# Kernel optimization log

Hardware: AMD Instinct MI355X
Metric: run time of the kernel (lower is better)

The kernel has to match this reference:

```python
import jax, jax.numpy as jnp
import numpy as np

N = 20000      # nodes
E = 640000     # edges
FIN = 256
FQK = 256


def setup_inputs() -> dict:
    key = jax.random.key(0)
    kx, ks, kd, kw = jax.random.split(key, 4)
    x = jax.random.normal(kx, (N, FIN), dtype=jnp.float32)
    # src must be sorted (original scatter_softmax assumes grouped index);
    # force last element to N-1 so nbatches == N as in batch[-1]+1.
    src = jnp.sort(jax.random.randint(ks, (E,), 0, N))
    src = src.at[-1].set(N - 1)
    dest = jax.random.randint(kd, (E,), 0, N)
    ei = jnp.stack([src, dest]).astype(jnp.int64)
    # nn.Linear(Fin, 2*Fqk, bias=False) weight: [2*Fqk, Fin]
    bound = 1.0 / np.sqrt(FIN)
    W = jax.random.uniform(kw, (2 * FQK, FIN), dtype=jnp.float32,
                           minval=-bound, maxval=bound)
    return {"x": x, "ei": ei, "W": W}


def reference(x, ei, W):
    src, dest = ei[0], ei[1]
    n_nodes = x.shape[0]
    scaling = FQK ** -0.5
    qk = x @ W.T                      # [N, 2*Fqk]
    q, k = jnp.split(qk, 2, axis=-1)  # each [N, Fqk]
    q = q * scaling
    # per-edge dot product: (q[src] . k[dest])  -> [E]
    aw = jnp.einsum('ef,ef->e', q[src], k[dest])
    # scatter softmax over edges grouped by src node (raw exp, as original)
    ex = jnp.exp(aw)
    expsum = jax.ops.segment_sum(ex, src, num_segments=n_nodes)  # [N]
    return ex / expsum[src]
```

## Files before the change

### kernel.cpp

```cpp
#include <hip/hip_runtime.h>
#include <cmath>

#define FIN 256
#define FQK 256
#define SCALING 0.0625f
#define ASTRIDE 264

typedef _Float16 f16_t;
typedef f16_t f16x8 __attribute__((ext_vector_type(8)));
typedef f16_t f16x2 __attribute__((ext_vector_type(2)));
typedef float f32x4 __attribute__((ext_vector_type(4)));

__device__ __forceinline__ f16x8 cvt8h(float4 a, float4 b) {
    f16x8 r;
    r[0] = (f16_t)a.x; r[1] = (f16_t)a.y; r[2] = (f16_t)a.z; r[3] = (f16_t)a.w;
    r[4] = (f16_t)b.x; r[5] = (f16_t)b.y; r[6] = (f16_t)b.z; r[7] = (f16_t)b.w;
    return r;
}

__device__ __forceinline__ float fdot2f(f16x2 a, f16x2 b, float c) {
#if __has_builtin(__builtin_amdgcn_fdot2)
    return __builtin_amdgcn_fdot2(a, b, c, false);
#else
    return c + (float)a[0] * (float)b[0] + (float)a[1] * (float)b[1];
#endif
}

union H16 { uint4 u; f16x2 h[4]; };
__device__ __forceinline__ float dot16(uint4 ya, uint4 xa, float acc) {
    H16 A; A.u = ya;
    H16 X; X.u = xa;
#pragma unroll
    for (int i = 0; i < 4; ++i) acc = fdot2f(A.h[i], X.h[i], acc);
    return acc;
}

__global__ __launch_bounds__(256) void m_seg_kernel(const float* __restrict__ W,
                                                    f16_t* __restrict__ MbF,
                                                    const int* __restrict__ src,
                                                    int* __restrict__ seg, int N, int E) {
    const int b = blockIdx.x;
    if (b < FIN) {
        const int f = b;
        const int k = threadIdx.x;
        const float* __restrict__ Wq = W;
        const float* __restrict__ Wk = W + FQK * FIN;
        float acc = 0.f;
#pragma unroll 8
        for (int c = 0; c < FQK; ++c)
            acc += Wq[c * FIN + f] * Wk[c * FIN + k];
        const int ft  = f >> 4, m16 = f & 15;
        const int kcI = k >> 5, q = (k >> 3) & 3, e = k & 7;
        MbF[(size_t)(((kcI * 16 + ft) * 64 + q * 16 + m16) * 8 + e)] =
            (f16_t)(acc * SCALING);
    } else {
        const int n = (b - FIN) * 256 + threadIdx.x;
        if (n > N) return;
        int lo = 0, hi = E;
        while (lo < hi) {
            const int mid = (lo + hi) >> 1;
            if (src[mid] < n) lo = mid + 1; else hi = mid;
        }
        seg[n] = lo;
    }
}

__global__ __launch_bounds__(256) void gemm_y_kernel(const float* __restrict__ x,
                                                     const f16_t* __restrict__ MbF,
                                                     f16_t* __restrict__ y,
                                                     f16_t* __restrict__ xh, int N) {
    __shared__ f16_t sA[16 * ASTRIDE];

    const int t    = threadIdx.x;
    const int wv   = t >> 6;
    const int lane = t & 63;
    const int q    = lane >> 4;
    const int m16  = lane & 15;
    const int n0   = blockIdx.x * 16;
    const int f0   = wv * 64;

    {
        const int rsub = t >> 5;
        const int col  = (t & 31) * 8;
#pragma unroll
        for (int p = 0; p < 2; ++p) {
            const int r  = p * 8 + rsub;
            const int n  = n0 + r;
            const int nc = n < N ? n : N - 1;
            const float* __restrict__ xp = x + (size_t)nc * FIN + col;
            const float4 a = *(const float4*)(xp);
            const float4 b = *(const float4*)(xp + 4);
            const f16x8 v = cvt8h(a, b);
            *(f16x8*)&sA[r * ASTRIDE + col] = v;
            if (n < N) *(f16x8*)(xh + (size_t)n * FIN + col) = v;
        }
    }
    __syncthreads();

    f32x4 acc[4] = {};

#pragma unroll
    for (int kc = 0; kc < FIN; kc += 32) {
        const f16x8 af = *(const f16x8*)&sA[m16 * ASTRIDE + kc + q * 8];
        const f16_t* __restrict__ bp =
            MbF + (size_t)(((kc >> 5) * 16 + (f0 >> 4)) * 64 + lane) * 8;
#pragma unroll
        for (int ft = 0; ft < 4; ++ft) {
            union { uint4 u; f16x8 v; } bu;
            bu.u = *(const uint4*)(bp + ft * 512);
            acc[ft] = __builtin_amdgcn_mfma_f32_16x16x32_f16(af, bu.v, acc[ft], 0, 0, 0);
        }
    }

    __syncthreads();
#pragma unroll
    for (int ft = 0; ft < 4; ++ft)
#pragma unroll
        for (int r = 0; r < 4; ++r)
            sA[(q * 4 + r) * ASTRIDE + f0 + ft * 16 + m16] = (f16_t)acc[ft][r];
    __syncthreads();

    {
        const int row = t >> 4;
        const int c   = (t & 15) * 16;
        const int n   = n0 + row;
        if (n < N) {
            const uint4 v0 = *(const uint4*)&sA[row * ASTRIDE + c];
            const uint4 v1 = *(const uint4*)&sA[row * ASTRIDE + c + 8];
            *(uint4*)(y + (size_t)n * FIN + c)     = v0;
            *(uint4*)(y + (size_t)n * FIN + c + 8) = v1;
        }
    }
}

__global__ __launch_bounds__(256) void edge_dot_kernel(const f16_t* __restrict__ xh,
                                                       const f16_t* __restrict__ y,
                                                       const int* __restrict__ src,
                                                       const int* __restrict__ dest,
                                                       float* __restrict__ out,
                                                       int N, int E, int span) {
    const int w    = threadIdx.x >> 6;
    const int lane = threadIdx.x & 63;
    const int g    = lane >> 3;
    const int j    = lane & 7;

    const int base = (blockIdx.x * 4 + w) * span;
    if (base >= E) return;
    const int end = min(base + span, E);

#define ECLAMP(d, L) ((unsigned)(d) < (unsigned)(L) ? (d) : 0)

#define EISSUE(Y0, Y1, Y2, Y3, X0, X1, X2, X3, e, valid)                       \
    if (valid) {                                                               \
        const int d_ = ECLAMP(dest[e], N);                                     \
        const int s_ = ECLAMP(src[e], N);                                      \
        const uint4* __restrict__ yr = (const uint4*)(y + (size_t)d_ * FIN) + j * 4;  \
        const uint4* __restrict__ xr = (const uint4*)(xh + (size_t)s_ * FIN) + j * 4; \
        Y0 = yr[0]; Y1 = yr[1]; Y2 = yr[2]; Y3 = yr[3];                        \
        X0 = xr[0]; X1 = xr[1]; X2 = xr[2]; X3 = xr[3];                        \
    }

#define ECONSUME(Y0, Y1, Y2, Y3, X0, X1, X2, X3, e, valid)                     \
    if (valid) {                                                               \
        float a_ = 0.f;                                                        \
        a_ = dot16(Y0, X0, a_);                                                \
        a_ = dot16(Y1, X1, a_);                                                \
        a_ = dot16(Y2, X2, a_);                                                \
        a_ = dot16(Y3, X3, a_);                                                \
        a_ += __shfl_xor(a_, 1, 64);                                           \
        a_ += __shfl_xor(a_, 2, 64);                                           \
        a_ += __shfl_xor(a_, 4, 64);                                           \
        if (j == 0) out[e] = __expf(a_);                                       \
    }

    uint4 A0, A1, A2, A3, AX0, AX1, AX2, AX3;
    uint4 B0, B1, B2, B3, BX0, BX1, BX2, BX3;

    int  eA = base + g;
    bool vA = eA < end;
    EISSUE(A0, A1, A2, A3, AX0, AX1, AX2, AX3, eA, vA);

    const int nit = (end - base + 7) >> 3;
    for (int it = 0; it < nit; it += 2) {
        const int eB = base + (it + 1) * 8 + g;
        const bool vB = eB < end;
        EISSUE(B0, B1, B2, B3, BX0, BX1, BX2, BX3, eB, vB);
        ECONSUME(A0, A1, A2, A3, AX0, AX1, AX2, AX3, eA, vA);
        eA = base + (it + 2) * 8 + g;
        vA = eA < end;
        EISSUE(A0, A1, A2, A3, AX0, AX1, AX2, AX3, eA, vA);
        ECONSUME(B0, B1, B2, B3, BX0, BX1, BX2, BX3, eB, vB);
    }

#undef EISSUE
#undef ECONSUME
#undef ECLAMP
}

__global__ __launch_bounds__(256) void segnorm_kernel(float* __restrict__ out,
                                                      const int* __restrict__ seg,
                                                      int N, int E) {
    const int n = blockIdx.x * 32 + (threadIdx.x >> 3);
    const int j = threadIdx.x & 7;
    if (n >= N) return;

    int s0 = seg[n], s1 = seg[n + 1];
    s0 = min(max(s0, 0), E);
    s1 = min(max(s1, 0), E);
    if (s1 <= s0) return;

    float sum = 0.f;
    for (int i = s0 + j; i < s1; i += 8) sum += out[i];
    sum += __shfl_xor(sum, 1, 64);
    sum += __shfl_xor(sum, 2, 64);
    sum += __shfl_xor(sum, 4, 64);
    const float inv = 1.0f / sum;

    for (int i = s0 + j; i < s1; i += 8) out[i] *= inv;
}

extern "C" void kernel_launch(void* const* d_in, const int* in_sizes, int n_in,
                              void* d_out, int out_size, void* d_ws, size_t ws_size,
                              hipStream_t stream) {
    const float* x  = (const float*)d_in[0];
    const int*   ei = (const int*)d_in[1];
    const float* W  = (const float*)d_in[2];
    float* out = (float*)d_out;

    const int N = in_sizes[0] / FIN;
    const int E = in_sizes[1] / 2;

    f16_t* MbF = (f16_t*)d_ws;
    f16_t* y   = MbF + (size_t)FIN * FIN;
    f16_t* xh  = y + (size_t)N * FIN;
    int*   seg = (int*)(xh + (size_t)N * FIN);

    const int segBlocks = (N + 256) / 256;
    m_seg_kernel<<<FIN + segBlocks, 256, 0, stream>>>(W, MbF, ei, seg, N, E);

    gemm_y_kernel<<<(N + 15) / 16, 256, 0, stream>>>(x, MbF, y, xh, N);

    const int neBlocks = 1024;
    const int nwaves   = neBlocks * 4;
    const int span     = ((E + nwaves - 1) / nwaves + 7) & ~7;
    edge_dot_kernel<<<neBlocks, 256, 0, stream>>>(xh, y, ei, ei + E, out, N, E, span);

    segnorm_kernel<<<(N + 31) / 32, 256, 0, stream>>>(out, seg, N, E);
}
```

Before: 145.3 us.

## Bucket edges by destination range to improve y-row cache locality in edge dot

Adds a counting pass and a single-block prefix scan that partition edges into 8 buckets by destination node range, then scatters (src, dest) pairs and an original-index permutation into bucket order inside the GEMM launch. The edge-dot kernel assigns blocks to buckets so each group of waves gathers y rows from a narrower node range, aiming for better L2/LLC reuse of the random dest gathers. It also changes the per-lane load pattern to interleaved uint4 reads across the row. The cost is an extra kernel launch, atomics-based scatter traffic, and scattered writes to out through perm.

```diff
diff --git a/kernel.cpp b/kernel.cpp
--- a/kernel.cpp
+++ b/kernel.cpp
@@ -5,6 +5,8 @@
 #define FQK 256
 #define SCALING 0.0625f
 #define ASTRIDE 264
+#define NBUCKET 8
+#define CHUNK 512
 
 typedef _Float16 f16_t;
 typedef f16_t f16x8 __attribute__((ext_vector_type(8)));
@@ -35,14 +37,20 @@
     return acc;
 }
 
-__global__ __launch_bounds__(256) void m_seg_kernel(const float* __restrict__ W,
-                                                    f16_t* __restrict__ MbF,
-                                                    const int* __restrict__ src,
-                                                    int* __restrict__ seg, int N, int E) {
+__global__ __launch_bounds__(256) void m_seg_count_kernel(const float* __restrict__ W,
+                                                          f16_t* __restrict__ MbF,
+                                                          const int* __restrict__ src,
+                                                          const int* __restrict__ dest,
+                                                          int* __restrict__ seg,
+                                                          int* __restrict__ counts,
+                                                          int N, int E, int segB, int NC,
+                                                          int SLICE) {
+    __shared__ int cnt8[NBUCKET];
     const int b = blockIdx.x;
+    const int t = threadIdx.x;
     if (b < FIN) {
         const int f = b;
-        const int k = threadIdx.x;
+        const int k = t;
         const float* __restrict__ Wq = W;
         const float* __restrict__ Wk = W + FQK * FIN;
         float acc = 0.f;
@@ -53,8 +61,8 @@
         const int kcI = k >> 5, q = (k >> 3) & 3, e = k & 7;
         MbF[(size_t)(((kcI * 16 + ft) * 64 + q * 16 + m16) * 8 + e)] =
             (f16_t)(acc * SCALING);
-    } else {
-        const int n = (b - FIN) * 256 + threadIdx.x;
+    } else if (b < FIN + segB) {
+        const int n = (b - FIN) * 256 + t;
         if (n > N) return;
         int lo = 0, hi = E;
         while (lo < hi) {
@@ -62,16 +70,102 @@
             if (src[mid] < n) lo = mid + 1; else hi = mid;
         }
         seg[n] = lo;
-    }
-}
-
-__global__ __launch_bounds__(256) void gemm_y_kernel(const float* __restrict__ x,
-                                                     const f16_t* __restrict__ MbF,
-                                                     f16_t* __restrict__ y,
-                                                     f16_t* __restrict__ xh, int N) {
+    } else {
+        const int c = b - FIN - segB;
+        if (t < NBUCKET) cnt8[t] = 0;
+        __syncthreads();
+#pragma unroll
+        for (int u = 0; u < 2; ++u) {
+            const int e = c * CHUNK + u * 256 + t;
+            if (e < E) {
+                int d = dest[e];
+                d = ((unsigned)d < (unsigned)N) ? d : 0;
+                const int bk = min(d / SLICE, NBUCKET - 1);
+                atomicAdd(&cnt8[bk], 1);
+            }
+        }
+        __syncthreads();
+        if (t < NBUCKET) counts[c * NBUCKET + t] = cnt8[t];
+    }
+}
+
+__global__ __launch_bounds__(256) void prefix_kernel(const int* __restrict__ counts,
+                                                     int* __restrict__ cbase,
+                                                     int* __restrict__ bstart,
+                                                     int NC, int E) {
+    __shared__ int part[256];
+    const int t = threadIdx.x;
+    const int K = NBUCKET * NC;
+    const int per = (K + 255) / 256;
+    const int L0 = t * per;
+
+    int s = 0;
+    for (int i = 0; i < per; ++i) {
+        const int L = L0 + i;
+        if (L < K) {
+            const int bk = L / NC, c = L % NC;
+            s += counts[c * NBUCKET + bk];
+        }
+    }
+    int val = s;
+    part[t] = val;
+    __syncthreads();
+    for (int off = 1; off < 256; off <<= 1) {
+        const int add = (t >= off) ? part[t - off] : 0;
+        __syncthreads();
+        val += add;
+        part[t] = val;
+        __syncthreads();
+    }
+    int p = val - s;
+    for (int i = 0; i < per; ++i) {
+        const int L = L0 + i;
+        if (L < K) {
+            const int bk = L / NC, c = L % NC;
+            if (c == 0) bstart[bk] = p;
+            cbase[c * NBUCKET + bk] = p;
+            p += counts[c * NBUCKET + bk];
+        }
+    }
+    if (t == 0) bstart[NBUCKET] = E;
+}
+
+__global__ __launch_bounds__(256) void gemm_scatter_kernel(const float* __restrict__ x,
+                                                           const f16_t* __restrict__ MbF,
+                                                           f16_t* __restrict__ y,
+                                                           f16_t* __restrict__ xh,
+                                                           const int* __restrict__ src,
+                                                           const int* __restrict__ dest,
+                                                           const int* __restrict__ cbase,
+                                                           uint2* __restrict__ sd2,
+                                                           int* __restrict__ perm,
+                                                           int N, int E, int GB, int SLICE) {
+    const int t = threadIdx.x;
+    if (blockIdx.x >= GB) {
+        __shared__ int off8[NBUCKET];
+        const int c = blockIdx.x - GB;
+        if (t < NBUCKET) off8[t] = cbase[c * NBUCKET + t];
+        __syncthreads();
+#pragma unroll
+        for (int u = 0; u < 2; ++u) {
+            const int e = c * CHUNK + u * 256 + t;
+            if (e < E) {
+                int d = dest[e];
+                d = ((unsigned)d < (unsigned)N) ? d : 0;
+                int s = src[e];
+                s = ((unsigned)s < (unsigned)N) ? s : 0;
+                const int bk = min(d / SLICE, NBUCKET - 1);
+                const int p  = atomicAdd(&off8[bk], 1);
+                if ((unsigned)p < (unsigned)E) {
+                    sd2[p]  = make_uint2((unsigned)s, (unsigned)d);
+                    perm[p] = e;
+                }
+            }
+        }
+        return;
+    }
+
     __shared__ f16_t sA[16 * ASTRIDE];
-
-    const int t    = threadIdx.x;
     const int wv   = t >> 6;
     const int lane = t & 63;
     const int q    = lane >> 4;
@@ -89,8 +183,8 @@
             const int nc = n < N ? n : N - 1;
             const float* __restrict__ xp = x + (size_t)nc * FIN + col;
             const float4 a = *(const float4*)(xp);
-            const float4 b = *(const float4*)(xp + 4);
-            const f16x8 v = cvt8h(a, b);
+            const float4 b2 = *(const float4*)(xp + 4);
+            const f16x8 v = cvt8h(a, b2);
             *(f16x8*)&sA[r * ASTRIDE + col] = v;
             if (n < N) *(f16x8*)(xh + (size_t)n * FIN + col) = v;
         }
@@ -98,7 +192,6 @@
     __syncthreads();
 
     f32x4 acc[4] = {};
-
 #pragma unroll
     for (int kc = 0; kc < FIN; kc += 32) {
         const f16x8 af = *(const f16x8*)&sA[m16 * ASTRIDE + kc + q * 8];
@@ -135,32 +228,40 @@
 
 __global__ __launch_bounds__(256) void edge_dot_kernel(const f16_t* __restrict__ xh,
                                                        const f16_t* __restrict__ y,
-                                                       const int* __restrict__ src,
-                                                       const int* __restrict__ dest,
+                                                       const uint2* __restrict__ sd2,
+                                                       const int* __restrict__ perm,
+                                                       const int* __restrict__ bstart,
                                                        float* __restrict__ out,
-                                                       int N, int E, int span) {
+                                                       int N, int E) {
     const int w    = threadIdx.x >> 6;
     const int lane = threadIdx.x & 63;
     const int g    = lane >> 3;
     const int j    = lane & 7;
 
-    const int base = (blockIdx.x * 4 + w) * span;
-    if (base >= E) return;
-    const int end = min(base + span, E);
-
-#define ECLAMP(d, L) ((unsigned)(d) < (unsigned)(L) ? (d) : 0)
-
-#define EISSUE(Y0, Y1, Y2, Y3, X0, X1, X2, X3, e, valid)                       \
+    const int bk  = blockIdx.x & 7;
+    const int wib = (blockIdx.x >> 3) * 4 + w;
+    const int nw  = (gridDim.x >> 3) * 4;
+
+    int lo = bstart[bk], hi = bstart[bk + 1];
+    lo = min(max(lo, 0), E);
+    hi = min(max(hi, lo), E);
+    const int len = hi - lo;
+    if (len <= 0) return;
+    const int spanw = ((len + nw - 1) / nw + 7) & ~7;
+    const int base  = lo + wib * spanw;
+    if (base >= hi) return;
+    const int end = min(base + spanw, hi);
+
+#define EISSUE(Y0, Y1, Y2, Y3, X0, X1, X2, X3, pe, valid)                      \
     if (valid) {                                                               \
-        const int d_ = ECLAMP(dest[e], N);                                     \
-        const int s_ = ECLAMP(src[e], N);                                      \
-        const uint4* __restrict__ yr = (const uint4*)(y + (size_t)d_ * FIN) + j * 4;  \
-        const uint4* __restrict__ xr = (const uint4*)(xh + (size_t)s_ * FIN) + j * 4; \
-        Y0 = yr[0]; Y1 = yr[1]; Y2 = yr[2]; Y3 = yr[3];                        \
-        X0 = xr[0]; X1 = xr[1]; X2 = xr[2]; X3 = xr[3];                        \
-    }
-
-#define ECONSUME(Y0, Y1, Y2, Y3, X0, X1, X2, X3, e, valid)                     \
+        const uint2 sd = sd2[pe];                                              \
+        const uint4* __restrict__ yr = (const uint4*)(y + (size_t)sd.y * FIN); \
+        const uint4* __restrict__ xr = (const uint4*)(xh + (size_t)sd.x * FIN);\
+        Y0 = yr[j]; Y1 = yr[8 + j]; Y2 = yr[16 + j]; Y3 = yr[24 + j];          \
+        X0 = xr[j]; X1 = xr[8 + j]; X2 = xr[16 + j]; X3 = xr[24 + j];          \
+    }
+
+#define ECONSUME(Y0, Y1, Y2, Y3, X0, X1, X2, X3, pe, valid)                    \
     if (valid) {                                                               \
         float a_ = 0.f;                                                        \
         a_ = dot16(Y0, X0, a_);                                                \
@@ -170,7 +271,10 @@
         a_ += __shfl_xor(a_, 1, 64);                                           \
         a_ += __shfl_xor(a_, 2, 64);                                           \
         a_ += __shfl_xor(a_, 4, 64);                                           \
-        if (j == 0) out[e] = __expf(a_);                                       \
+        if (j == 0) {                                                          \
+            const int oe = perm[pe];                                           \
+            if ((unsigned)oe < (unsigned)E) out[oe] = __expf(a_);              \
+        }                                                                      \
     }
 
     uint4 A0, A1, A2, A3, AX0, AX1, AX2, AX3;
@@ -194,7 +298,6 @@
 
 #undef EISSUE
 #undef ECONSUME
-#undef ECLAMP
 }
 
 __global__ __launch_bounds__(256) void segnorm_kernel(float* __restrict__ out,
@@ -229,21 +332,30 @@
 
     const int N = in_sizes[0] / FIN;
     const int E = in_sizes[1] / 2;
+    const int SLICE = (N + NBUCKET - 1) / NBUCKET;
+    const int NC = (E + CHUNK - 1) / CHUNK;
 
     f16_t* MbF = (f16_t*)d_ws;
     f16_t* y   = MbF + (size_t)FIN * FIN;
     f16_t* xh  = y + (size_t)N * FIN;
-    int*   seg = (int*)(xh + (size_t)N * FIN);
-
-    const int segBlocks = (N + 256) / 256;
-    m_seg_kernel<<<FIN + segBlocks, 256, 0, stream>>>(W, MbF, ei, seg, N, E);
-
-    gemm_y_kernel<<<(N + 15) / 16, 256, 0, stream>>>(x, MbF, y, xh, N);
-
-    const int neBlocks = 1024;
-    const int nwaves   = neBlocks * 4;
-    const int span     = ((E + nwaves - 1) / nwaves + 7) & ~7;
-    edge_dot_kernel<<<neBlocks, 256, 0, stream>>>(xh, y, ei, ei + E, out, N, E, span);
+    uint2* sd2 = (uint2*)(xh + (size_t)N * FIN);
+    int*   perm   = (int*)(sd2 + (size_t)E);
+    int*   seg    = perm + (size_t)E;
+    int*   counts = seg + (size_t)(N + 2);
+    int*   cbase  = counts + (size_t)NC * NBUCKET;
+    int*   bstart = cbase + (size_t)NC * NBUCKET;
+
+    const int segB = (N + 256) / 256;
+    m_seg_count_kernel<<<FIN + segB + NC, 256, 0, stream>>>(W, MbF, ei, ei + E, seg,
+                                                            counts, N, E, segB, NC, SLICE);
+
+    prefix_kernel<<<1, 256, 0, stream>>>(counts, cbase, bstart, NC, E);
+
+    const int GB = (N + 15) / 16;
+    gemm_scatter_kernel<<<GB + NC, 256, 0, stream>>>(x, MbF, y, xh, ei, ei + E,
+                                                     cbase, sd2, perm, N, E, GB, SLICE);
+
+    edge_dot_kernel<<<2048, 256, 0, stream>>>(xh, y, sd2, perm, bstart, out, N, E);
 
     segnorm_kernel<<<(N + 31) / 32, 256, 0, stream>>>(out, seg, N, E);
 }
```

New measurement: 157.4 us. 8.3% more time.
